# Performance work log

Measured on AMD Instinct MI355X. Metric: run time of the kernel, lower is better.

The kernel has to match this reference:

```python
import jax, jax.numpy as jnp
import numpy as np

EMBED_DIM = 1024
N_HEAD = 16

def setup_inputs() -> dict:
    key = jax.random.key(0)
    ks = jax.random.split(key, 5)
    C = EMBED_DIM
    x = jax.random.normal(ks[0], (2, 2048, C), dtype=jnp.float32)
    s = 1.0 / np.sqrt(C)
    W_attn = jax.random.normal(ks[1], (C, 3 * C), dtype=jnp.float32) * s
    b_attn = jnp.zeros((3 * C,), dtype=jnp.float32)
    W_proj = jax.random.normal(ks[2], (C, C), dtype=jnp.float32) * s
    b_proj = jnp.zeros((C,), dtype=jnp.float32)
    return {"x": x, "W_attn": W_attn, "b_attn": b_attn, "W_proj": W_proj, "b_proj": b_proj}

def reference(x, W_attn, b_attn, W_proj, b_proj):
    B, T, C = x.shape
    H = N_HEAD
    D = C // H
    qkv = x @ W_attn + b_attn                      # [B,T,3C]
    q, k, v = jnp.split(qkv, 3, axis=-1)
    # [B,H,T,D]
    q = q.reshape(B, T, H, D).transpose(0, 2, 1, 3)
    k = k.reshape(B, T, H, D).transpose(0, 2, 1, 3)
    v = v.reshape(B, T, H, D).transpose(0, 2, 1, 3)
    att = jnp.einsum('bhqd,bhkd->bhqk', q, k) * (1.0 / jnp.sqrt(jnp.asarray(D, x.dtype)))
    causal = jnp.tril(jnp.ones((T, T), dtype=bool))
    att = jnp.where(causal, att, -jnp.inf)
    att = jax.nn.softmax(att, axis=-1)
    y = jnp.einsum('bhqk,bhkd->bhqd', att, v)      # [B,H,T,D]
    y = y.transpose(0, 2, 1, 3).reshape(B, T, C)
    return y @ W_proj + b_proj
```

## Files before the change

kernel.cpp:

```cpp
#include <hip/hip_runtime.h>
#include <stdint.h>

typedef __attribute__((ext_vector_type(4))) float f32x4;
typedef __attribute__((ext_vector_type(8))) __bf16 bf16x8;
typedef __attribute__((ext_vector_type(8))) unsigned short u16x8;

__device__ __forceinline__ unsigned short f2b(float f) {
  unsigned u = __float_as_uint(f);
  u += 0x7FFFu + ((u >> 16) & 1u);
  return (unsigned short)(u >> 16);
}
__device__ __forceinline__ float b2f(unsigned short s) {
  unsigned u = (unsigned)s << 16;
  return __uint_as_float(u);
}
__device__ __forceinline__ unsigned cvtpk_bf16(float lo, float hi) {
  unsigned r;
  asm("v_cvt_pk_bf16_f32 %0, %1, %2" : "=v"(r) : "v"(lo), "v"(hi));
  return r;
}

__device__ __forceinline__ void gload_lds16(const void* g, void* l) {
  typedef __attribute__((address_space(1))) void GV1;
  typedef __attribute__((address_space(3))) void LV3;
  __builtin_amdgcn_global_load_lds((GV1*)(void*)g, (LV3*)l, 16, 0, 0);
}

__global__ __launch_bounds__(256) void convert_f32_bf16(const float* __restrict__ in,
                                                        unsigned short* __restrict__ out, int n) {
  int i = (blockIdx.x * 256 + threadIdx.x) * 8;
  if (i >= n) return;
  float4 a = *(const float4*)(in + i);
  float4 b = *(const float4*)(in + i + 4);
  u16x8 r;
  r[0] = f2b(a.x); r[1] = f2b(a.y); r[2] = f2b(a.z); r[3] = f2b(a.w);
  r[4] = f2b(b.x); r[5] = f2b(b.y); r[6] = f2b(b.z); r[7] = f2b(b.w);
  *(u16x8*)(out + i) = r;
}

__global__ __launch_bounds__(256) void transpose_f32_bf16(const float* __restrict__ W,
                                                          unsigned short* __restrict__ Wt,
                                                          int K, int N) {
  __shared__ unsigned short tile[32][33];
  int n0 = blockIdx.x * 32, k0 = blockIdx.y * 32;
  int tx = threadIdx.x, ty = threadIdx.y;
  #pragma unroll
  for (int j = 0; j < 32; j += 8)
    tile[ty + j][tx] = f2b(W[(size_t)(k0 + ty + j) * N + n0 + tx]);
  __syncthreads();
  #pragma unroll
  for (int j = 0; j < 32; j += 8)
    Wt[(size_t)(n0 + ty + j) * K + k0 + tx] = tile[tx][ty + j];
}

template <bool OUT_BF16, bool VSPLIT>
__global__ __launch_bounds__(256) void gemm_bt(const unsigned short* __restrict__ A,
                                               const unsigned short* __restrict__ Bt,
                                               const float* __restrict__ bias,
                                               void* __restrict__ Cout,
                                               unsigned short* __restrict__ vT,
                                               int M, int N, int K) {
  __shared__ unsigned short SMEM[128 * 136];
  unsigned short* As = SMEM;
  unsigned short* Bs = SMEM + 8192;
  const int m0 = blockIdx.x * 128, n0 = blockIdx.y * 128;
  const int tid = threadIdx.x;
  const int w = tid >> 6, l = tid & 63;
  const int wm = w >> 1, wn = w & 1;
  const int c = l & 15, g = l >> 4;
  f32x4 acc[4][4] = {};
  for (int k0 = 0; k0 < K; k0 += 64) {
    #pragma unroll
    for (int i = 0; i < 4; ++i) {
      int rb = w * 32 + i * 8;
      gload_lds16(A + (size_t)(m0 + rb + (l >> 3)) * K + k0 + (l & 7) * 8, &As[rb * 64]);
      gload_lds16(Bt + (size_t)(n0 + rb + (l >> 3)) * K + k0 + (l & 7) * 8, &Bs[rb * 64]);
    }
    __syncthreads();
    #pragma unroll
    for (int ks = 0; ks < 2; ++ks) {
      bf16x8 af[4], bf[4];
      #pragma unroll
      for (int mi = 0; mi < 4; ++mi)
        af[mi] = *(const bf16x8*)&As[(wm * 64 + mi * 16 + c) * 64 + ks * 32 + g * 8];
      #pragma unroll
      for (int ni = 0; ni < 4; ++ni)
        bf[ni] = *(const bf16x8*)&Bs[(wn * 64 + ni * 16 + c) * 64 + ks * 32 + g * 8];
      #pragma unroll
      for (int mi = 0; mi < 4; ++mi)
        #pragma unroll
        for (int ni = 0; ni < 4; ++ni)
          acc[mi][ni] = __builtin_amdgcn_mfma_f32_16x16x32_bf16(af[mi], bf[ni], acc[mi][ni], 0, 0, 0);
    }
    __syncthreads();
  }
  if (VSPLIT && n0 >= 2048) {
    #pragma unroll
    for (int mi = 0; mi < 4; ++mi)
      #pragma unroll
      for (int ni = 0; ni < 4; ++ni) {
        int cl = wn * 64 + ni * 16 + c;
        float bv = bias[n0 + cl];
        #pragma unroll
        for (int r = 0; r < 4; ++r) {
          int rl = wm * 64 + mi * 16 + 4 * g + r;
          SMEM[cl * 136 + rl] = f2b(acc[mi][ni][r] + bv);
        }
      }
    __syncthreads();
    const int d0 = n0 - 2048;
    #pragma unroll
    for (int p = 0; p < 8; ++p) {
      int rowl = p * 16 + (tid >> 4);
      *(u16x8*)(vT + (size_t)(d0 + rowl) * 4096 + m0 + (tid & 15) * 8) =
          *(const u16x8*)&SMEM[rowl * 136 + (tid & 15) * 8];
    }
    return;
  }
  const int NS = VSPLIT ? 2048 : N;
  #pragma unroll
  for (int mi = 0; mi < 4; ++mi) {
    #pragma unroll
    for (int ni = 0; ni < 4; ++ni) {
      int colg = n0 + wn * 64 + ni * 16 + c;
      float bv = bias[colg];
      #pragma unroll
      for (int r = 0; r < 4; ++r) {
        int rowg = m0 + wm * 64 + mi * 16 + 4 * g + r;
        float v = acc[mi][ni][r] + bv;
        if (OUT_BF16)
          ((unsigned short*)Cout)[(size_t)rowg * NS + colg] = f2b(v);
        else
          ((float*)Cout)[(size_t)rowg * NS + colg] = v;
      }
    }
  }
}

__global__ __launch_bounds__(512) void attn_kernel(const unsigned short* __restrict__ qk,
                                                   const unsigned short* __restrict__ vT,
                                                   unsigned short* __restrict__ partO,
                                                   float* __restrict__ partML) {
  __shared__ unsigned short K_lds[2][64 * 64];
  __shared__ unsigned short V_lds[2][64 * 64];
  const int bid = blockIdx.x;
  const int bh = bid & 31;
  const int cid = 39 - (bid >> 5);
  int qt, ct;
  if (cid < 4)       { qt = cid;            ct = 0; }
  else if (cid < 12) { int e = cid - 4;  qt = 4 + (e >> 1);  ct = e & 1; }
  else if (cid < 24) { int e = cid - 12; int q3 = e / 3; qt = 8 + q3; ct = e - 3 * q3; }
  else               { int e = cid - 24; qt = 12 + (e >> 2); ct = e & 3; }
  const int ntt = 2 * qt + 2;
  const int t0 = ct * 8;
  const int ntl = min(ntt - t0, 8);
  const int b = bh >> 4, h = bh & 15;
  const int tid = threadIdx.x, w = tid >> 6, l = tid & 63;
  const int c = l & 15, g = l >> 4;
  const int hi = g >> 1;
  const int srcA = c + ((g & 1) << 5);
  const int srcB = srcA + 16;
  const size_t row0 = (size_t)b * 2048;
  const float SCL = 0.18033688f;
  const int KSTRIDE = 64 * 2048;
  const int VSTRIDE = 64;

  const int q0w = qt * 128 + w * 16;
  const int qg = q0w + c;

  bf16x8 qf[2];
  #pragma unroll
  for (int ks = 0; ks < 2; ++ks)
    qf[ks] = *(const bf16x8*)(qk + (row0 + qg) * 2048 + h * 64 + ks * 32 + g * 8);

  f32x4 acc[4] = {};
  float mstate = -1e30f, lstate = 0.f;

  const int krow = w * 8 + (l >> 3);
  const int kch = (l & 7) ^ (krow & 7);
  const unsigned short* kptr = qk + (row0 + t0 * 64 + krow) * 2048 + 1024 + h * 64 + kch * 8;
  const unsigned short* vptr = vT + (size_t)(h * 64 + krow) * 4096 + (b * 2048 + t0 * 64) + kch * 8;
  const int kdst = (w * 8) * 64;

  gload_lds16(kptr, &K_lds[0][kdst]);
  gload_lds16(vptr, &V_lds[0][kdst]);
  __syncthreads();

  for (int lt = 0; lt < ntl; ++lt) {
    const int cur = lt & 1;
    const int kv0 = (t0 + lt) * 64;
    const bool pre = (lt + 1 < ntl);
    if (pre) {
      gload_lds16(kptr + KSTRIDE, &K_lds[cur ^ 1][kdst]);
      gload_lds16(vptr + VSTRIDE, &V_lds[cur ^ 1][kdst]);
    }
    kptr += KSTRIDE;
    vptr += VSTRIDE;
    if (kv0 <= q0w + 15) {
      const char* Kb = (const char*)K_lds[cur];
      const char* Vb = (const char*)V_lds[cur];
      f32x4 s[4] = {};
      #pragma unroll
      for (int ks = 0; ks < 2; ++ks) {
        bf16x8 kf[4];
        #pragma unroll
        for (int nk = 0; nk < 4; ++nk) {
          int row = nk * 16 + c;
          kf[nk] = *(const bf16x8*)(Kb + row * 128 + ((ks * 64 + g * 16) ^ ((row & 7) << 4)));
        }
        __builtin_amdgcn_s_setprio(1);
        #pragma unroll
        for (int nk = 0; nk < 4; ++nk)
          s[nk] = __builtin_amdgcn_mfma_f32_16x16x32_bf16(kf[nk], qf[ks], s[nk], 0, 0, 0);
        __builtin_amdgcn_s_setprio(0);
      }
      if (kv0 + 63 > q0w) {
        #pragma unroll
        for (int nk = 0; nk < 4; ++nk)
          #pragma unroll
          for (int r = 0; r < 4; ++r) {
            int kvg = kv0 + nk * 16 + 4 * g + r;
            if (kvg > qg) s[nk][r] = -1e30f;
          }
      }
      float a0 = fmaxf(fmaxf(s[0][0], s[0][1]), fmaxf(s[0][2], s[0][3]));
      float a1 = fmaxf(fmaxf(s[1][0], s[1][1]), fmaxf(s[1][2], s[1][3]));
      float a2 = fmaxf(fmaxf(s[2][0], s[2][1]), fmaxf(s[2][2], s[2][3]));
      float a3 = fmaxf(fmaxf(s[3][0], s[3][1]), fmaxf(s[3][2], s[3][3]));
      float mx = fmaxf(fmaxf(a0, a1), fmaxf(a2, a3));
      mx = fmaxf(mx, __shfl_xor(mx, 16));
      mx = fmaxf(mx, __shfl_xor(mx, 32));
      if (!__all(mx <= mstate)) {
        float mnew = fmaxf(mstate, mx);
        float alpha = exp2f((mstate - mnew) * SCL);
        mstate = mnew;
        lstate *= alpha;
        #pragma unroll
        for (int nd = 0; nd < 4; ++nd) acc[nd] *= alpha;
      }
      float ms = mstate * SCL;
      #pragma unroll
      for (int nk = 0; nk < 4; ++nk) {
        #pragma unroll
        for (int r = 0; r < 4; ++r) s[nk][r] = exp2f(fmaf(s[nk][r], SCL, -ms));
        lstate += (s[nk][0] + s[nk][1]) + (s[nk][2] + s[nk][3]);
      }
      unsigned pk[4][2];
      #pragma unroll
      for (int nk = 0; nk < 4; ++nk) {
        pk[nk][0] = cvtpk_bf16(s[nk][0], s[nk][1]);
        pk[nk][1] = cvtpk_bf16(s[nk][2], s[nk][3]);
      }
      #pragma unroll
      for (int vks = 0; vks < 2; ++vks) {
        unsigned rA00 = __shfl(pk[2 * vks][0], srcA, 64);
        unsigned rA01 = __shfl(pk[2 * vks][1], srcA, 64);
        unsigned rA10 = __shfl(pk[2 * vks + 1][0], srcA, 64);
        unsigned rA11 = __shfl(pk[2 * vks + 1][1], srcA, 64);
        unsigned rB00 = __shfl(pk[2 * vks][0], srcB, 64);
        unsigned rB01 = __shfl(pk[2 * vks][1], srcB, 64);
        unsigned rB10 = __shfl(pk[2 * vks + 1][0], srcB, 64);
        unsigned rB11 = __shfl(pk[2 * vks + 1][1], srcB, 64);
        union { unsigned u[4]; bf16x8 v; } pa;
        pa.u[0] = hi ? rA10 : rA00;
        pa.u[1] = hi ? rA11 : rA01;
        pa.u[2] = hi ? rB10 : rB00;
        pa.u[3] = hi ? rB11 : rB01;
        bf16x8 vf[4];
        #pragma unroll
        for (int nd = 0; nd < 4; ++nd) {
          int row = nd * 16 + c;
          vf[nd] = *(const bf16x8*)(Vb + row * 128 + ((vks * 64 + g * 16) ^ ((row & 7) << 4)));
        }
        __builtin_amdgcn_s_setprio(1);
        #pragma unroll
        for (int nd = 0; nd < 4; ++nd)
          acc[nd] = __builtin_amdgcn_mfma_f32_16x16x32_bf16(vf[nd], pa.v, acc[nd], 0, 0, 0);
        __builtin_amdgcn_s_setprio(0);
      }
    }
    __syncthreads();
  }

  float lsum = lstate;
  lsum += __shfl_xor(lsum, 16);
  lsum += __shfl_xor(lsum, 32);
  const int qrow = w * 16 + c;
  #pragma unroll
  for (int nd = 0; nd < 4; ++nd) {
    ushort4 o4;
    o4.x = f2b(acc[nd][0]); o4.y = f2b(acc[nd][1]);
    o4.z = f2b(acc[nd][2]); o4.w = f2b(acc[nd][3]);
    *(ushort4*)(partO + (size_t)bid * 8192 + qrow * 64 + nd * 16 + 4 * g) = o4;
  }
  if (g == 0) {
    partML[(size_t)bid * 256 + qrow * 2 + 0] = mstate;
    partML[(size_t)bid * 256 + qrow * 2 + 1] = lsum;
  }
}

__global__ __launch_bounds__(256) void attn_combine(const unsigned short* __restrict__ partO,
                                                    const float* __restrict__ partML,
                                                    unsigned short* __restrict__ out) {
  const int bid = blockIdx.x;
  const int qt = bid >> 5, bh = bid & 31;
  const int b = bh >> 4, h = bh & 15;
  const int np = (2 * qt + 9) >> 3;
  const int base = (qt < 4) ? qt
                 : (qt < 8) ? 4 + 2 * (qt - 4)
                 : (qt < 12) ? 12 + 3 * (qt - 8)
                 : 24 + 4 * (qt - 12);
  const int t = threadIdx.x;
  const int row = t >> 1, cg = (t & 1) * 32;
  const float SCL = 0.18033688f;
  float mstar = -1e30f;
  #pragma unroll
  for (int p = 0; p < 4; ++p)
    if (p < np)
      mstar = fmaxf(mstar, partML[(size_t)(((39 - (base + p)) << 5) | bh) * 256 + row * 2]);
  float L = 0.f;
  float o[32];
  #pragma unroll
  for (int j = 0; j < 32; ++j) o[j] = 0.f;
  #pragma unroll
  for (int p = 0; p < 4; ++p) {
    if (p < np) {
      int slot = ((39 - (base + p)) << 5) | bh;
      float mp = partML[(size_t)slot * 256 + row * 2 + 0];
      float lp = partML[(size_t)slot * 256 + row * 2 + 1];
      float wgt = exp2f((mp - mstar) * SCL);
      L = fmaf(wgt, lp, L);
      const unsigned short* src = partO + (size_t)slot * 8192 + row * 64 + cg;
      #pragma unroll
      for (int q = 0; q < 4; ++q) {
        u16x8 a = *(const u16x8*)(src + q * 8);
        #pragma unroll
        for (int j = 0; j < 8; ++j)
          o[q * 8 + j] = fmaf(b2f(a[j]), wgt, o[q * 8 + j]);
      }
    }
  }
  float rinv = 1.0f / L;
  size_t trow = (size_t)b * 2048 + qt * 128 + row;
  #pragma unroll
  for (int q = 0; q < 4; ++q) {
    u16x8 r;
    #pragma unroll
    for (int j = 0; j < 8; ++j) r[j] = f2b(o[q * 8 + j] * rinv);
    *(u16x8*)(out + trow * 1024 + h * 64 + cg + q * 8) = r;
  }
}

extern "C" void kernel_launch(void* const* d_in, const int* in_sizes, int n_in,
                              void* d_out, int out_size, void* d_ws, size_t ws_size,
                              hipStream_t stream) {
  const float* x      = (const float*)d_in[0];
  const float* W_attn = (const float*)d_in[1];
  const float* b_attn = (const float*)d_in[2];
  const float* W_proj = (const float*)d_in[3];
  const float* b_proj = (const float*)d_in[4];
  float* out = (float*)d_out;

  char* ws = (char*)d_ws;
  unsigned short* Wproj_t  = (unsigned short*)(ws + 0);
  unsigned short* qk       = (unsigned short*)(ws + 2097152);
  unsigned short* vT       = (unsigned short*)(ws + 18874368);
  unsigned short* x_bf     = (unsigned short*)(ws + 27262976);
  unsigned short* Wattn_t  = (unsigned short*)(ws + 35651584);
  unsigned short* partO    = (unsigned short*)(ws + 27262976);
  unsigned short* attn_out = (unsigned short*)(ws + 48234496);
  float*          partML   = (float*)(ws + 56623104);

  convert_f32_bf16<<<2048, 256, 0, stream>>>(x, x_bf, 4194304);
  transpose_f32_bf16<<<dim3(96, 32), dim3(32, 8), 0, stream>>>(W_attn, Wattn_t, 1024, 3072);
  transpose_f32_bf16<<<dim3(32, 32), dim3(32, 8), 0, stream>>>(W_proj, Wproj_t, 1024, 1024);

  gemm_bt<true, true><<<dim3(32, 24), 256, 0, stream>>>(x_bf, Wattn_t, b_attn, qk, vT,
                                                        4096, 3072, 1024);
  attn_kernel<<<1280, 512, 0, stream>>>(qk, vT, partO, partML);
  attn_combine<<<512, 256, 0, stream>>>(partO, partML, attn_out);
  gemm_bt<false, false><<<dim3(32, 8), 256, 0, stream>>>(attn_out, Wproj_t, b_proj, out, nullptr,
                                                         4096, 1024, 1024);
}
```

Measured before the change: 148.4 us.

## Double-buffer GEMM LDS tiles and use 512-thread blocks with setprio around MFMAs

The bf16 GEMM kernels now prefetch the next K-tile into a second LDS buffer while computing the current one. That removes one barrier per iteration and overlaps global-to-LDS loads with MFMA work. Blocks grow from 4 to 8 waves, so each wave owns a 64x32 sub-tile, and s_setprio raises priority around the MFMA burst. The V-transpose epilogue writes packed ushort4 values. LDS use doubles to 64KB per block, which may limit occupancy, and each wave does less MFMA work per LDS load.

New measurement: 137.1 us. 1.08x faster.

```diff
diff --git a/kernel.cpp b/kernel.cpp
--- a/kernel.cpp
+++ b/kernel.cpp
@@ -54,66 +54,89 @@
 }
 
 template <bool OUT_BF16, bool VSPLIT>
-__global__ __launch_bounds__(256) void gemm_bt(const unsigned short* __restrict__ A,
+__global__ __launch_bounds__(512) void gemm_bt(const unsigned short* __restrict__ A,
                                                const unsigned short* __restrict__ Bt,
                                                const float* __restrict__ bias,
                                                void* __restrict__ Cout,
                                                unsigned short* __restrict__ vT,
                                                int M, int N, int K) {
-  __shared__ unsigned short SMEM[128 * 136];
-  unsigned short* As = SMEM;
-  unsigned short* Bs = SMEM + 8192;
+  __shared__ unsigned short SMEM[32768];
   const int m0 = blockIdx.x * 128, n0 = blockIdx.y * 128;
   const int tid = threadIdx.x;
   const int w = tid >> 6, l = tid & 63;
-  const int wm = w >> 1, wn = w & 1;
+  const int wm = w >> 2, wn = w & 3;
   const int c = l & 15, g = l >> 4;
-  f32x4 acc[4][4] = {};
-  for (int k0 = 0; k0 < K; k0 += 64) {
-    #pragma unroll
-    for (int i = 0; i < 4; ++i) {
-      int rb = w * 32 + i * 8;
-      gload_lds16(A + (size_t)(m0 + rb + (l >> 3)) * K + k0 + (l & 7) * 8, &As[rb * 64]);
-      gload_lds16(Bt + (size_t)(n0 + rb + (l >> 3)) * K + k0 + (l & 7) * 8, &Bs[rb * 64]);
-    }
-    __syncthreads();
+  const int NT = K >> 6;
+  const unsigned short* aptr[2];
+  const unsigned short* bptr[2];
+  #pragma unroll
+  for (int i = 0; i < 2; ++i) {
+    int rb = w * 16 + i * 8;
+    aptr[i] = A  + (size_t)(m0 + rb + (l >> 3)) * K + (l & 7) * 8;
+    bptr[i] = Bt + (size_t)(n0 + rb + (l >> 3)) * K + (l & 7) * 8;
+  }
+  f32x4 acc[4][2] = {};
+  #pragma unroll
+  for (int i = 0; i < 2; ++i) {
+    int rb = w * 16 + i * 8;
+    gload_lds16(aptr[i], &SMEM[rb * 64]);
+    gload_lds16(bptr[i], &SMEM[8192 + rb * 64]);
+  }
+  __syncthreads();
+  for (int t = 0; t < NT; ++t) {
+    const int cur = t & 1;
+    const unsigned short* Ab = &SMEM[cur * 16384];
+    const unsigned short* Bb = &SMEM[cur * 16384 + 8192];
+    if (t + 1 < NT) {
+      unsigned short* An = &SMEM[(cur ^ 1) * 16384];
+      unsigned short* Bn = &SMEM[(cur ^ 1) * 16384 + 8192];
+      #pragma unroll
+      for (int i = 0; i < 2; ++i) {
+        int rb = w * 16 + i * 8;
+        gload_lds16(aptr[i] + (size_t)(t + 1) * 64, &An[rb * 64]);
+        gload_lds16(bptr[i] + (size_t)(t + 1) * 64, &Bn[rb * 64]);
+      }
+    }
     #pragma unroll
     for (int ks = 0; ks < 2; ++ks) {
-      bf16x8 af[4], bf[4];
+      bf16x8 af[4], bf[2];
       #pragma unroll
       for (int mi = 0; mi < 4; ++mi)
-        af[mi] = *(const bf16x8*)&As[(wm * 64 + mi * 16 + c) * 64 + ks * 32 + g * 8];
-      #pragma unroll
-      for (int ni = 0; ni < 4; ++ni)
-        bf[ni] = *(const bf16x8*)&Bs[(wn * 64 + ni * 16 + c) * 64 + ks * 32 + g * 8];
+        af[mi] = *(const bf16x8*)&Ab[(wm * 64 + mi * 16 + c) * 64 + ks * 32 + g * 8];
+      #pragma unroll
+      for (int ni = 0; ni < 2; ++ni)
+        bf[ni] = *(const bf16x8*)&Bb[(wn * 32 + ni * 16 + c) * 64 + ks * 32 + g * 8];
+      __builtin_amdgcn_s_setprio(1);
       #pragma unroll
       for (int mi = 0; mi < 4; ++mi)
         #pragma unroll
-        for (int ni = 0; ni < 4; ++ni)
+        for (int ni = 0; ni < 2; ++ni)
           acc[mi][ni] = __builtin_amdgcn_mfma_f32_16x16x32_bf16(af[mi], bf[ni], acc[mi][ni], 0, 0, 0);
+      __builtin_amdgcn_s_setprio(0);
     }
     __syncthreads();
   }
   if (VSPLIT && n0 >= 2048) {
+    unsigned short* TR = SMEM;
     #pragma unroll
     for (int mi = 0; mi < 4; ++mi)
       #pragma unroll
-      for (int ni = 0; ni < 4; ++ni) {
-        int cl = wn * 64 + ni * 16 + c;
+      for (int ni = 0; ni < 2; ++ni) {
+        int cl = wn * 32 + ni * 16 + c;
         float bv = bias[n0 + cl];
-        #pragma unroll
-        for (int r = 0; r < 4; ++r) {
-          int rl = wm * 64 + mi * 16 + 4 * g + r;
-          SMEM[cl * 136 + rl] = f2b(acc[mi][ni][r] + bv);
-        }
+        int rlb = wm * 64 + mi * 16 + 4 * g;
+        ushort4 o4;
+        o4.x = f2b(acc[mi][ni][0] + bv); o4.y = f2b(acc[mi][ni][1] + bv);
+        o4.z = f2b(acc[mi][ni][2] + bv); o4.w = f2b(acc[mi][ni][3] + bv);
+        *(ushort4*)&TR[cl * 136 + rlb] = o4;
       }
     __syncthreads();
     const int d0 = n0 - 2048;
     #pragma unroll
-    for (int p = 0; p < 8; ++p) {
-      int rowl = p * 16 + (tid >> 4);
+    for (int p = 0; p < 4; ++p) {
+      int rowl = p * 32 + (tid >> 4);
       *(u16x8*)(vT + (size_t)(d0 + rowl) * 4096 + m0 + (tid & 15) * 8) =
-          *(const u16x8*)&SMEM[rowl * 136 + (tid & 15) * 8];
+          *(const u16x8*)&TR[rowl * 136 + (tid & 15) * 8];
     }
     return;
   }
@@ -121,8 +144,8 @@
   #pragma unroll
   for (int mi = 0; mi < 4; ++mi) {
     #pragma unroll
-    for (int ni = 0; ni < 4; ++ni) {
-      int colg = n0 + wn * 64 + ni * 16 + c;
+    for (int ni = 0; ni < 2; ++ni) {
+      int colg = n0 + wn * 32 + ni * 16 + c;
       float bv = bias[colg];
       #pragma unroll
       for (int r = 0; r < 4; ++r) {
@@ -375,10 +398,10 @@
   transpose_f32_bf16<<<dim3(96, 32), dim3(32, 8), 0, stream>>>(W_attn, Wattn_t, 1024, 3072);
   transpose_f32_bf16<<<dim3(32, 32), dim3(32, 8), 0, stream>>>(W_proj, Wproj_t, 1024, 1024);
 
-  gemm_bt<true, true><<<dim3(32, 24), 256, 0, stream>>>(x_bf, Wattn_t, b_attn, qk, vT,
+  gemm_bt<true, true><<<dim3(32, 24), 512, 0, stream>>>(x_bf, Wattn_t, b_attn, qk, vT,
                                                         4096, 3072, 1024);
   attn_kernel<<<1280, 512, 0, stream>>>(qk, vT, partO, partML);
   attn_combine<<<512, 256, 0, stream>>>(partO, partML, attn_out);
-  gemm_bt<false, false><<<dim3(32, 8), 256, 0, stream>>>(attn_out, Wproj_t, b_proj, out, nullptr,
+  gemm_bt<false, false><<<dim3(32, 8), 512, 0, stream>>>(attn_out, Wproj_t, b_proj, out, nullptr,
                                                          4096, 1024, 1024);
 }
```
